# Kernel optimization log

Measured on AMD Instinct MI355X. Metric: run time of the kernel, lower is better.

Reference implementation:

```python
import jax, jax.numpy as jnp
import numpy as np

B, N, E = 16, 5000, 160000
IN, OUT, H = 64, 64, 1  # heads=1 (GATConv default)
NEG_SLOPE = 0.2


def setup_inputs() -> dict:
    key = jax.random.key(0)
    ks = jax.random.split(key, 10)
    data = jax.random.normal(ks[0], (B, N, IN), jnp.float32)
    # random edges with no self-loops (PyG removes then re-adds self-loops;
    # with no pre-existing self-loops this matches exactly)
    src = jax.random.randint(ks[1], (E,), 0, N)
    off = jax.random.randint(ks[2], (E,), 1, N)
    dst = (src + off) % N
    edge_index = jnp.stack([src, dst]).astype(jnp.int32)
    edge_attr = jax.random.uniform(ks[3], (E,), jnp.float32)
    # GATConv parameters (glorot-ish init)
    W = jax.random.normal(ks[4], (H * OUT, IN), jnp.float32) / np.sqrt(IN)
    W_edge = jax.random.normal(ks[5], (H * OUT, 1), jnp.float32)
    att_src = jax.random.normal(ks[6], (1, H, OUT), jnp.float32) * 0.1
    att_dst = jax.random.normal(ks[7], (1, H, OUT), jnp.float32) * 0.1
    att_edge = jax.random.normal(ks[8], (1, H, OUT), jnp.float32) * 0.1
    bias = jnp.zeros((H * OUT,), jnp.float32)
    return {"data": data, "edge_index": edge_index, "edge_attr": edge_attr,
            "W": W, "W_edge": W_edge, "att_src": att_src, "att_dst": att_dst,
            "att_edge": att_edge, "bias": bias}


def reference(data, edge_index, edge_attr, W, W_edge, att_src, att_dst, att_edge, bias):
    BN = B * N
    x = data.reshape(BN, IN)
    # faithful to source: tile edges per batch WITHOUT node offset
    ei = jnp.tile(edge_index, (1, B))          # [2, B*E]
    ea = jnp.tile(edge_attr, B)[:, None]        # [B*E, 1]
    # add self-loops for all BN nodes, edge_attr filled with mean
    loops = jnp.arange(BN, dtype=ei.dtype)
    src = jnp.concatenate([ei[0], loops])       # [Etot]
    dst = jnp.concatenate([ei[1], loops])
    ea = jnp.concatenate([ea, jnp.full((BN, 1), ea.mean(), ea.dtype)])
    # linear transforms
    xl = (x @ W.T).reshape(BN, H, OUT)          # [BN, H, C]
    a_src = (xl * att_src).sum(-1)              # [BN, H]
    a_dst = (xl * att_dst).sum(-1)
    e_emb = (ea @ W_edge.T).reshape(-1, H, OUT) # [Etot, H, C]
    a_edge = (e_emb * att_edge).sum(-1)         # [Etot, H]
    # per-edge attention + segment softmax over destination nodes
    alpha = a_src[src] + a_dst[dst] + a_edge
    alpha = jax.nn.leaky_relu(alpha, NEG_SLOPE)
    amax = jax.ops.segment_max(alpha, dst, num_segments=BN)
    alpha = jnp.exp(alpha - amax[dst])
    denom = jax.ops.segment_sum(alpha, dst, num_segments=BN)
    alpha = alpha / (denom[dst] + 1e-16)
    # message passing: gather src features, weight, scatter-sum to dst
    msg = xl[src] * alpha[:, :, None]           # [Etot, H, C]
    out = jax.ops.segment_sum(msg, dst, num_segments=BN)
    out = out.reshape(BN, H * OUT) + bias
    return out.reshape(B, N, OUT), jnp.stack([src, dst]), alpha
```

## Files before the change

kernel.cpp:

```cpp
#include <hip/hip_runtime.h>

#define NN 5000
#define EE 160000
#define BB 16
#define BNN 80000
#define BEE 2560000
#define ETOT 2640000
#define CAP 128

typedef __attribute__((ext_vector_type(8))) short short8;
typedef __attribute__((ext_vector_type(4))) float floatx4;

__device__ __forceinline__ short8 pack_bf8(const float* p) {
    union { unsigned int u[4]; short8 s; } r;
    #pragma unroll
    for (int j = 0; j < 4; ++j) {
        unsigned int lo = __float_as_uint(p[2 * j]) >> 16;
        unsigned int hi = __float_as_uint(p[2 * j + 1]) & 0xFFFF0000u;
        r.u[j] = lo | hi;
    }
    return r.s;
}

__global__ __launch_bounds__(256) void k_pre(
        const float* __restrict__ ea, const float* __restrict__ wedge,
        const float* __restrict__ atte,
        int* __restrict__ cursor, float* __restrict__ partials) {
    __shared__ float red[256];
    int t = threadIdx.x;
    int gid = blockIdx.x * 256 + t;
    if (gid < NN) cursor[gid] = 0;
    float v = 0.f;
    for (int i = gid; i < EE; i += 20 * 256) v += ea[i];
    red[t] = v;
    __syncthreads();
    #pragma unroll
    for (int off = 128; off > 0; off >>= 1) {
        if (t < off) red[t] += red[t + off];
        __syncthreads();
    }
    if (t == 0) partials[blockIdx.x] = red[0];
    if (blockIdx.x == 0 && t < 64) {
        float s = wedge[t] * atte[t];
        #pragma unroll
        for (int off = 32; off > 0; off >>= 1) s += __shfl_xor(s, off, 64);
        if (t == 0) partials[20] = s;
    }
}

__global__ void k_fill(const int* __restrict__ ei,
                       int* __restrict__ cursor, int* __restrict__ bucket) {
    int e = blockIdx.x * 256 + threadIdx.x;
    int d = ei[EE + e];
    int pos = atomicAdd(&cursor[d], 1);
    if (pos < CAP) bucket[d * CAP + pos] = e;
}

__global__ __launch_bounds__(256) void k1_gemm(
        const float* __restrict__ x,
        const float* __restrict__ W,
        const float* __restrict__ att_src,
        const float* __restrict__ att_dst,
        const float* __restrict__ bias,
        float* __restrict__ xl, float* __restrict__ asrc, float* __restrict__ adst,
        float* __restrict__ out0) {
    const int wave = threadIdx.x >> 6;
    const int lane = threadIdx.x & 63;
    const int quad = lane >> 4;
    const int col  = lane & 15;

    short8 bfrag[4][2];
    float attsv[4], attdv[4], biasv[4];
    #pragma unroll
    for (int ct = 0; ct < 4; ++ct) {
        int c = ct * 16 + col;
        #pragma unroll
        for (int ks = 0; ks < 2; ++ks)
            bfrag[ct][ks] = pack_bf8(W + c * 64 + ks * 32 + quad * 8);
        attsv[ct] = att_src[c];
        attdv[ct] = att_dst[c];
        biasv[ct] = bias[c];
    }

    int node0 = (blockIdx.x * 4 + wave) << 4;
    short8 afrag[2];
    const float* xrow = x + (size_t)(node0 + col) * 64;
    #pragma unroll
    for (int ks = 0; ks < 2; ++ks)
        afrag[ks] = pack_bf8(xrow + ks * 32 + quad * 8);
    floatx4 acc[4];
    #pragma unroll
    for (int ct = 0; ct < 4; ++ct) acc[ct] = (floatx4){0.f, 0.f, 0.f, 0.f};
    #pragma unroll
    for (int ks = 0; ks < 2; ++ks)
        #pragma unroll
        for (int ct = 0; ct < 4; ++ct)
            acc[ct] = __builtin_amdgcn_mfma_f32_16x16x32_bf16(afrag[ks], bfrag[ct][ks], acc[ct], 0, 0, 0);

    float ps[4] = {0.f,0.f,0.f,0.f}, pd[4] = {0.f,0.f,0.f,0.f};
    #pragma unroll
    for (int r = 0; r < 4; ++r) {
        int node = node0 + quad * 4 + r;
        #pragma unroll
        for (int ct = 0; ct < 4; ++ct) {
            float v = acc[ct][r];
            out0[node * 64 + ct * 16 + col] = v + biasv[ct];
            if (node < NN) xl[node * 64 + ct * 16 + col] = v;
            ps[r] += v * attsv[ct];
            pd[r] += v * attdv[ct];
        }
    }
    #pragma unroll
    for (int off = 1; off < 16; off <<= 1) {
        #pragma unroll
        for (int r = 0; r < 4; ++r) {
            ps[r] += __shfl_xor(ps[r], off, 64);
            pd[r] += __shfl_xor(pd[r], off, 64);
        }
    }
    if (col == 0) {
        #pragma unroll
        for (int r = 0; r < 4; ++r) {
            int node = node0 + quad * 4 + r;
            if (node < NN) { asrc[node] = ps[r]; adst[node] = pd[r]; }
        }
    }
}

__global__ __launch_bounds__(256) void k_gather(
        const int* __restrict__ ei, const float* __restrict__ ea,
        const int* __restrict__ bucket, const int* __restrict__ cursor,
        const float* __restrict__ asrc, const float* __restrict__ adst,
        const float* __restrict__ partials,
        const float* __restrict__ xl, const float* __restrict__ bias,
        float* __restrict__ albuf, float* __restrict__ selfal,
        float* __restrict__ out0) {
    __shared__ float s_r[4][CAP];
    __shared__ int   s_se[4][CAP];
    __shared__ int   s_e[4][CAP];
    int wave = threadIdx.x >> 6, lane = threadIdx.x & 63;
    int d = blockIdx.x * 4 + wave;
    int deg = min(cursor[d], CAP);
    float s0 = 0.f;
    #pragma unroll
    for (int i = 0; i < 20; ++i) s0 += partials[i];
    float s1 = partials[20];
    float mean = s0 * (1.0f / EE);
    float ad = adst[d];
    float rs = asrc[d] + ad + mean * s1;
    rs = (rs > 0.f) ? rs : 0.2f * rs;
    float rmax = rs;
    for (int base = 0; base < deg; base += 64) {
        int idx = base + lane;
        if (idx < deg) {
            int e  = bucket[d * CAP + idx];
            int se = ei[e];
            float r = asrc[se] + ad + ea[e] * s1;
            r = (r > 0.f) ? r : 0.2f * r;
            s_r[wave][idx] = r; s_se[wave][idx] = se; s_e[wave][idx] = e;
            rmax = fmaxf(rmax, r);
        }
    }
    #pragma unroll
    for (int off = 32; off > 0; off >>= 1) rmax = fmaxf(rmax, __shfl_xor(rmax, off, 64));
    float m = rmax;
    float es = __expf(rs - m);
    float l = es;
    float acc = es * xl[d * 64 + lane];
    int j = 0;
    for (; j + 4 <= deg; j += 4) {
        int se0 = s_se[wave][j],     se1 = s_se[wave][j + 1];
        int se2 = s_se[wave][j + 2], se3 = s_se[wave][j + 3];
        float x0 = xl[se0 * 64 + lane], x1 = xl[se1 * 64 + lane];
        float x2 = xl[se2 * 64 + lane], x3 = xl[se3 * 64 + lane];
        float w0 = __expf(s_r[wave][j]     - m), w1 = __expf(s_r[wave][j + 1] - m);
        float w2 = __expf(s_r[wave][j + 2] - m), w3 = __expf(s_r[wave][j + 3] - m);
        acc += 16.0f * (w0 * x0 + w1 * x1 + w2 * x2 + w3 * x3);
        l   += 16.0f * (w0 + w1 + w2 + w3);
    }
    for (; j < deg; ++j) {
        int se0 = s_se[wave][j];
        float w0 = __expf(s_r[wave][j] - m);
        acc += 16.0f * w0 * xl[se0 * 64 + lane];
        l   += 16.0f * w0;
    }
    float inv = 1.0f / (l + 1e-16f);
    out0[d * 64 + lane] = acc * inv + bias[lane];
    if (lane == 0) selfal[d] = es * inv;
    for (int idx = lane; idx < deg; idx += 64)
        albuf[s_e[wave][idx]] = __expf(s_r[wave][idx] - m) * inv;
}

__global__ void k6_edges(const int* __restrict__ ei,
                         const float* __restrict__ albuf,
                         const float* __restrict__ selfal,
                         float* __restrict__ out1, float* __restrict__ out2) {
    int i = blockIdx.x * 256 + threadIdx.x;
    if (i >= ETOT) return;
    float sf, df, alpha;
    if (i < BEE) {
        int oe = i % EE;
        sf = (float)ei[oe]; df = (float)ei[EE + oe];
        alpha = albuf[oe];
    } else {
        int dd = i - BEE;
        sf = df = (float)dd;
        alpha = (dd < NN) ? selfal[dd] : 1.0f;
    }
    out1[i] = sf;
    out1[ETOT + i] = df;
    out2[i] = alpha;
}

extern "C" void kernel_launch(void* const* d_in, const int* in_sizes, int n_in,
                              void* d_out, int out_size, void* d_ws, size_t ws_size,
                              hipStream_t stream) {
    const float* data  = (const float*)d_in[0];
    const int*   ei    = (const int*)d_in[1];
    const float* ea    = (const float*)d_in[2];
    const float* W     = (const float*)d_in[3];
    const float* wedge = (const float*)d_in[4];
    const float* atts  = (const float*)d_in[5];
    const float* attd  = (const float*)d_in[6];
    const float* atte  = (const float*)d_in[7];
    const float* bias  = (const float*)d_in[8];

    float* out0 = (float*)d_out;
    float* out1 = out0 + 5120000;
    float* out2 = out0 + 10400000;

    float* ws = (float*)d_ws;
    float* xl       = ws;
    float* asrc     = ws + 320000;
    float* adst     = ws + 325000;
    float* albuf    = ws + 330000;
    float* selfal   = ws + 490000;
    float* partials = ws + 495000;
    int*   cursor   = (int*)(ws + 495022);
    int*   bucket   = (int*)(ws + 500022);

    k_pre   <<<20,    256, 0, stream>>>(ea, wedge, atte, cursor, partials);
    k_fill  <<<625,   256, 0, stream>>>(ei, cursor, bucket);
    k1_gemm <<<1250,  256, 0, stream>>>(data, W, atts, attd, bias, xl, asrc, adst, out0);
    k_gather<<<1250,  256, 0, stream>>>(ei, ea, bucket, cursor, asrc, adst, partials,
                                        xl, bias, albuf, selfal, out0);
    k6_edges<<<10313, 256, 0, stream>>>(ei, albuf, selfal, out1, out2);
}
```

Baseline: 144.2 us.

## Fuse GEMM, edge-attr sum and index output into one mega kernel

Merges the edge-attr sum and cursor reset, the bf16 MFMA GEMM, and the edge-index float output into a single block-partitioned kernel. The partial-sum finalisation moves into an extra block of the bucket-fill kernel. The alpha output becomes a separate vectorised float4 grid-stride kernel. The aim is fewer launches and overlap of independent memory-bound work, with the index output written before the gather stage. The trade-off is more code branching, workspace offsets that change, and the extra partials block in k_fill racing with nothing only because launches are stream-ordered.

Measured after the change: 128.6 us. -10.8%, faster.

```diff
diff --git a/kernel.cpp b/kernel.cpp
--- a/kernel.cpp
+++ b/kernel.cpp
@@ -8,6 +8,11 @@
 #define ETOT 2640000
 #define CAP 128
 
+#define GEMM_BLKS 1250
+#define SUM_BLKS  80
+#define OUT1_BLKS 2578
+#define MEGA_BLKS (GEMM_BLKS + SUM_BLKS + OUT1_BLKS)
+
 typedef __attribute__((ext_vector_type(8))) short short8;
 typedef __attribute__((ext_vector_type(4))) float floatx4;
 
@@ -22,108 +27,140 @@
     return r.s;
 }
 
-__global__ __launch_bounds__(256) void k_pre(
+__global__ __launch_bounds__(256) void k_mega(
+        const float* __restrict__ x, const float* __restrict__ W,
+        const float* __restrict__ att_src, const float* __restrict__ att_dst,
+        const float* __restrict__ bias,
         const float* __restrict__ ea, const float* __restrict__ wedge,
-        const float* __restrict__ atte,
-        int* __restrict__ cursor, float* __restrict__ partials) {
+        const float* __restrict__ atte, const int* __restrict__ ei,
+        float* __restrict__ xl, float* __restrict__ asrc, float* __restrict__ adst,
+        float* __restrict__ out0,
+        int* __restrict__ cursor, float* __restrict__ partials,
+        float* __restrict__ out1) {
     __shared__ float red[256];
-    int t = threadIdx.x;
-    int gid = blockIdx.x * 256 + t;
-    if (gid < NN) cursor[gid] = 0;
-    float v = 0.f;
-    for (int i = gid; i < EE; i += 20 * 256) v += ea[i];
-    red[t] = v;
-    __syncthreads();
-    #pragma unroll
-    for (int off = 128; off > 0; off >>= 1) {
-        if (t < off) red[t] += red[t + off];
-        __syncthreads();
-    }
-    if (t == 0) partials[blockIdx.x] = red[0];
-    if (blockIdx.x == 0 && t < 64) {
-        float s = wedge[t] * atte[t];
-        #pragma unroll
-        for (int off = 32; off > 0; off >>= 1) s += __shfl_xor(s, off, 64);
-        if (t == 0) partials[20] = s;
-    }
-}
-
-__global__ void k_fill(const int* __restrict__ ei,
-                       int* __restrict__ cursor, int* __restrict__ bucket) {
-    int e = blockIdx.x * 256 + threadIdx.x;
-    int d = ei[EE + e];
-    int pos = atomicAdd(&cursor[d], 1);
-    if (pos < CAP) bucket[d * CAP + pos] = e;
-}
-
-__global__ __launch_bounds__(256) void k1_gemm(
-        const float* __restrict__ x,
-        const float* __restrict__ W,
-        const float* __restrict__ att_src,
-        const float* __restrict__ att_dst,
-        const float* __restrict__ bias,
-        float* __restrict__ xl, float* __restrict__ asrc, float* __restrict__ adst,
-        float* __restrict__ out0) {
-    const int wave = threadIdx.x >> 6;
-    const int lane = threadIdx.x & 63;
-    const int quad = lane >> 4;
-    const int col  = lane & 15;
-
-    short8 bfrag[4][2];
-    float attsv[4], attdv[4], biasv[4];
-    #pragma unroll
-    for (int ct = 0; ct < 4; ++ct) {
-        int c = ct * 16 + col;
+    const int blk = blockIdx.x;
+    const int t = threadIdx.x;
+
+    if (blk < GEMM_BLKS) {
+        const int wave = t >> 6;
+        const int lane = t & 63;
+        const int quad = lane >> 4;
+        const int col  = lane & 15;
+        short8 bfrag[4][2];
+        float attsv[4], attdv[4], biasv[4];
+        #pragma unroll
+        for (int ct = 0; ct < 4; ++ct) {
+            int c = ct * 16 + col;
+            #pragma unroll
+            for (int ks = 0; ks < 2; ++ks)
+                bfrag[ct][ks] = pack_bf8(W + c * 64 + ks * 32 + quad * 8);
+            attsv[ct] = att_src[c];
+            attdv[ct] = att_dst[c];
+            biasv[ct] = bias[c];
+        }
+        int node0 = (blk * 4 + wave) << 4;
+        short8 afrag[2];
+        const float* xrow = x + (size_t)(node0 + col) * 64;
         #pragma unroll
         for (int ks = 0; ks < 2; ++ks)
-            bfrag[ct][ks] = pack_bf8(W + c * 64 + ks * 32 + quad * 8);
-        attsv[ct] = att_src[c];
-        attdv[ct] = att_dst[c];
-        biasv[ct] = bias[c];
-    }
-
-    int node0 = (blockIdx.x * 4 + wave) << 4;
-    short8 afrag[2];
-    const float* xrow = x + (size_t)(node0 + col) * 64;
-    #pragma unroll
-    for (int ks = 0; ks < 2; ++ks)
-        afrag[ks] = pack_bf8(xrow + ks * 32 + quad * 8);
-    floatx4 acc[4];
-    #pragma unroll
-    for (int ct = 0; ct < 4; ++ct) acc[ct] = (floatx4){0.f, 0.f, 0.f, 0.f};
-    #pragma unroll
-    for (int ks = 0; ks < 2; ++ks)
-        #pragma unroll
-        for (int ct = 0; ct < 4; ++ct)
-            acc[ct] = __builtin_amdgcn_mfma_f32_16x16x32_bf16(afrag[ks], bfrag[ct][ks], acc[ct], 0, 0, 0);
-
-    float ps[4] = {0.f,0.f,0.f,0.f}, pd[4] = {0.f,0.f,0.f,0.f};
-    #pragma unroll
-    for (int r = 0; r < 4; ++r) {
-        int node = node0 + quad * 4 + r;
-        #pragma unroll
-        for (int ct = 0; ct < 4; ++ct) {
-            float v = acc[ct][r];
-            out0[node * 64 + ct * 16 + col] = v + biasv[ct];
-            if (node < NN) xl[node * 64 + ct * 16 + col] = v;
-            ps[r] += v * attsv[ct];
-            pd[r] += v * attdv[ct];
-        }
-    }
-    #pragma unroll
-    for (int off = 1; off < 16; off <<= 1) {
-        #pragma unroll
-        for (int r = 0; r < 4; ++r) {
-            ps[r] += __shfl_xor(ps[r], off, 64);
-            pd[r] += __shfl_xor(pd[r], off, 64);
-        }
-    }
-    if (col == 0) {
+            afrag[ks] = pack_bf8(xrow + ks * 32 + quad * 8);
+        floatx4 acc[4];
+        #pragma unroll
+        for (int ct = 0; ct < 4; ++ct) acc[ct] = (floatx4){0.f, 0.f, 0.f, 0.f};
+        #pragma unroll
+        for (int ks = 0; ks < 2; ++ks)
+            #pragma unroll
+            for (int ct = 0; ct < 4; ++ct)
+                acc[ct] = __builtin_amdgcn_mfma_f32_16x16x32_bf16(afrag[ks], bfrag[ct][ks], acc[ct], 0, 0, 0);
+        float ps[4] = {0.f,0.f,0.f,0.f}, pd[4] = {0.f,0.f,0.f,0.f};
         #pragma unroll
         for (int r = 0; r < 4; ++r) {
             int node = node0 + quad * 4 + r;
-            if (node < NN) { asrc[node] = ps[r]; adst[node] = pd[r]; }
-        }
+            #pragma unroll
+            for (int ct = 0; ct < 4; ++ct) {
+                float v = acc[ct][r];
+                out0[node * 64 + ct * 16 + col] = v + biasv[ct];
+                if (node < NN) xl[node * 64 + ct * 16 + col] = v;
+                ps[r] += v * attsv[ct];
+                pd[r] += v * attdv[ct];
+            }
+        }
+        #pragma unroll
+        for (int off = 1; off < 16; off <<= 1) {
+            #pragma unroll
+            for (int r = 0; r < 4; ++r) {
+                ps[r] += __shfl_xor(ps[r], off, 64);
+                pd[r] += __shfl_xor(pd[r], off, 64);
+            }
+        }
+        if (col == 0) {
+            #pragma unroll
+            for (int r = 0; r < 4; ++r) {
+                int node = node0 + quad * 4 + r;
+                if (node < NN) { asrc[node] = ps[r]; adst[node] = pd[r]; }
+            }
+        }
+    } else if (blk < GEMM_BLKS + SUM_BLKS) {
+        int sb = blk - GEMM_BLKS;
+        int gid = sb * 256 + t;
+        if (gid < NN) cursor[gid] = 0;
+        float v = 0.f;
+        for (int i = gid; i < EE; i += SUM_BLKS * 256) v += ea[i];
+        red[t] = v;
+        __syncthreads();
+        #pragma unroll
+        for (int off = 128; off > 0; off >>= 1) {
+            if (t < off) red[t] += red[t + off];
+            __syncthreads();
+        }
+        if (t == 0) partials[sb] = red[0];
+        if (sb == 0 && t < 64) {
+            float s = wedge[t] * atte[t];
+            #pragma unroll
+            for (int off = 32; off > 0; off >>= 1) s += __shfl_xor(s, off, 64);
+            if (t == 0) partials[80] = s;
+        }
+    } else {
+        int qb = blk - (GEMM_BLKS + SUM_BLKS);
+        for (int q = qb * 256 + t; q < ETOT / 4; q += OUT1_BLKS * 256) {
+            int i = q * 4;
+            float4 sv, dv;
+            if (i < BEE) {
+                int oe = i % EE;
+                int4 s4 = *reinterpret_cast<const int4*>(ei + oe);
+                int4 d4 = *reinterpret_cast<const int4*>(ei + EE + oe);
+                sv = make_float4((float)s4.x, (float)s4.y, (float)s4.z, (float)s4.w);
+                dv = make_float4((float)d4.x, (float)d4.y, (float)d4.z, (float)d4.w);
+            } else {
+                int nn = i - BEE;
+                sv = make_float4((float)nn, (float)(nn+1), (float)(nn+2), (float)(nn+3));
+                dv = sv;
+            }
+            *reinterpret_cast<float4*>(out1 + i) = sv;
+            *reinterpret_cast<float4*>(out1 + ETOT + i) = dv;
+        }
+    }
+}
+
+__global__ __launch_bounds__(256) void k_fill(const int* __restrict__ ei,
+                       int* __restrict__ cursor, int* __restrict__ bucket,
+                       float* __restrict__ partials) {
+    __shared__ float red[128];
+    int b = blockIdx.x, t = threadIdx.x;
+    if (b < 625) {
+        int e = b * 256 + t;
+        int d = ei[EE + e];
+        int pos = atomicAdd(&cursor[d], 1);
+        if (pos < CAP) bucket[d * CAP + pos] = e;
+    } else {
+        if (t < 128) red[t] = (t < 80) ? partials[t] : 0.f;
+        __syncthreads();
+        #pragma unroll
+        for (int off = 64; off > 0; off >>= 1) {
+            if (t < off) red[t] += red[t + off];
+            __syncthreads();
+        }
+        if (t == 0) { partials[81] = red[0]; partials[82] = partials[80]; }
     }
 }
 
@@ -141,11 +178,8 @@
     int wave = threadIdx.x >> 6, lane = threadIdx.x & 63;
     int d = blockIdx.x * 4 + wave;
     int deg = min(cursor[d], CAP);
-    float s0 = 0.f;
-    #pragma unroll
-    for (int i = 0; i < 20; ++i) s0 += partials[i];
-    float s1 = partials[20];
-    float mean = s0 * (1.0f / EE);
+    float s1 = partials[82];
+    float mean = partials[81] * (1.0f / EE);
     float ad = adst[d];
     float rs = asrc[d] + ad + mean * s1;
     rs = (rs > 0.f) ? rs : 0.2f * rs;
@@ -191,25 +225,26 @@
         albuf[s_e[wave][idx]] = __expf(s_r[wave][idx] - m) * inv;
 }
 
-__global__ void k6_edges(const int* __restrict__ ei,
-                         const float* __restrict__ albuf,
-                         const float* __restrict__ selfal,
-                         float* __restrict__ out1, float* __restrict__ out2) {
-    int i = blockIdx.x * 256 + threadIdx.x;
-    if (i >= ETOT) return;
-    float sf, df, alpha;
-    if (i < BEE) {
-        int oe = i % EE;
-        sf = (float)ei[oe]; df = (float)ei[EE + oe];
-        alpha = albuf[oe];
-    } else {
-        int dd = i - BEE;
-        sf = df = (float)dd;
-        alpha = (dd < NN) ? selfal[dd] : 1.0f;
-    }
-    out1[i] = sf;
-    out1[ETOT + i] = df;
-    out2[i] = alpha;
+__global__ void k_alpha(const float* __restrict__ albuf,
+                        const float* __restrict__ selfal,
+                        float* __restrict__ out2) {
+    int t = threadIdx.x;
+    for (int q = blockIdx.x * 256 + t; q < ETOT / 4; q += OUT1_BLKS * 256) {
+        int i = q * 4;
+        float4 av;
+        if (i < BEE) {
+            av = *reinterpret_cast<const float4*>(albuf + (i % EE));
+        } else {
+            float a[4];
+            #pragma unroll
+            for (int jj = 0; jj < 4; ++jj) {
+                int nn = i + jj - BEE;
+                a[jj] = (nn < NN) ? selfal[nn] : 1.0f;
+            }
+            av = make_float4(a[0], a[1], a[2], a[3]);
+        }
+        *reinterpret_cast<float4*>(out2 + i) = av;
+    }
 }
 
 extern "C" void kernel_launch(void* const* d_in, const int* in_sizes, int n_in,
@@ -236,13 +271,14 @@
     float* albuf    = ws + 330000;
     float* selfal   = ws + 490000;
     float* partials = ws + 495000;
-    int*   cursor   = (int*)(ws + 495022);
-    int*   bucket   = (int*)(ws + 500022);
-
-    k_pre   <<<20,    256, 0, stream>>>(ea, wedge, atte, cursor, partials);
-    k_fill  <<<625,   256, 0, stream>>>(ei, cursor, bucket);
-    k1_gemm <<<1250,  256, 0, stream>>>(data, W, atts, attd, bias, xl, asrc, adst, out0);
-    k_gather<<<1250,  256, 0, stream>>>(ei, ea, bucket, cursor, asrc, adst, partials,
-                                        xl, bias, albuf, selfal, out0);
-    k6_edges<<<10313, 256, 0, stream>>>(ei, albuf, selfal, out1, out2);
-}
+    int*   cursor   = (int*)(ws + 495084);
+    int*   bucket   = (int*)(ws + 500084);
+
+    k_mega  <<<MEGA_BLKS, 256, 0, stream>>>(data, W, atts, attd, bias, ea, wedge,
+                                            atte, ei, xl, asrc, adst, out0,
+                                            cursor, partials, out1);
+    k_fill  <<<626,       256, 0, stream>>>(ei, cursor, bucket, partials);
+    k_gather<<<1250,      256, 0, stream>>>(ei, ea, bucket, cursor, asrc, adst,
+                                            partials, xl, bias, albuf, selfal, out0);
+    k_alpha <<<OUT1_BLKS, 256, 0, stream>>>(albuf, selfal, out2);
+}
```
